# Performance work log

Measured on AMD Instinct MI355X. Metric: run time of the kernel, lower is better.

The kernel has to match this reference:

```python
import jax, jax.numpy as jnp
import numpy as np

N = 20000      # nodes
E = 320000     # edges (avg degree 16)
IN = 128       # in_size
H = 256        # layer_size
DEPTH = 2      # extra hidden layers
BN_EPS = 1e-5


def setup_inputs() -> dict:
    key = jax.random.key(0)
    ks = jax.random.split(key, 16)
    x = jax.random.normal(ks[0], (N, IN), jnp.float32)
    edge_index = jax.random.randint(ks[1], (2, E), 0, N)
    # first MLP layer: Linear(2*IN -> H) + BatchNorm1d(H) (inference stats)
    W0 = jax.random.normal(ks[2], (H, 2 * IN), jnp.float32) * 0.05
    b0 = jnp.zeros((H,), jnp.float32)
    g0 = jnp.ones((H,), jnp.float32)
    beta0 = jnp.zeros((H,), jnp.float32)
    m0 = jax.random.normal(ks[3], (H,), jnp.float32) * 0.1
    v0 = jax.random.uniform(ks[4], (H,), jnp.float32, 0.5, 1.5)
    # DEPTH repeated layers: Linear(H -> H) + BatchNorm1d(H)
    Ws = jax.random.normal(ks[5], (DEPTH, H, H), jnp.float32) * 0.05
    bs = jnp.zeros((DEPTH, H), jnp.float32)
    gs = jnp.ones((DEPTH, H), jnp.float32)
    betas = jnp.zeros((DEPTH, H), jnp.float32)
    ms = jax.random.normal(ks[6], (DEPTH, H), jnp.float32) * 0.1
    vs = jax.random.uniform(ks[7], (DEPTH, H), jnp.float32, 0.5, 1.5)
    return {"x": x, "edge_index": edge_index,
            "W0": W0, "b0": b0, "g0": g0, "beta0": beta0, "m0": m0, "v0": v0,
            "Ws": Ws, "bs": bs, "gs": gs, "betas": betas, "ms": ms, "vs": vs}


def _bn(h, g, b, m, v):
    # BatchNorm1d in inference mode (running stats)
    return (h - m) * (g * jax.lax.rsqrt(v + BN_EPS)) + b


def reference(x, edge_index, W0, b0, g0, beta0, m0, v0, Ws, bs, gs, betas, ms, vs):
    src = edge_index[0]  # x_j (source / neighbor)
    dst = edge_index[1]  # x_i (target), also scatter index
    # gather + concat: [E, 2*IN]
    h = jnp.concatenate([x[dst], x[src]], axis=-1)
    # edge MLP (dropout is identity in eval mode)
    h = jax.nn.selu(_bn(h @ W0.T + b0, g0, beta0, m0, v0))
    for i in range(DEPTH):
        h = jax.nn.selu(_bn(h @ Ws[i].T + bs[i], gs[i], betas[i], ms[i], vs[i]))
    # scatter-mean aggregation onto target nodes
    agg_sum = jax.ops.segment_sum(h, dst, num_segments=N)
    cnt = jax.ops.segment_sum(jnp.ones((E,), h.dtype), dst, num_segments=N)
    agg = agg_sum / jnp.maximum(cnt, 1.0)[:, None]
    return (agg, h)  # (aggregated node features, edge activations)
```

## Files before the change

### kernel.cpp

```cpp
#include <hip/hip_runtime.h>
#include <hip/hip_bf16.h>

#define IN_F 128
#define HF 256
#define BN_EPS 1e-5f
#define SELU_SCALE 1.0507009873554805f
#define SELU_ALPHA 1.6732632423543772f

typedef __attribute__((ext_vector_type(8))) _Float16 half8;
typedef __attribute__((ext_vector_type(2))) unsigned int u32x2;
typedef __attribute__((ext_vector_type(4))) float f32x4;

__device__ __forceinline__ short f2h(float f) {
    _Float16 h = (_Float16)f;
    return __builtin_bit_cast(short, h);
}

__device__ __forceinline__ float selu_f(float x) {
    const float SA = SELU_SCALE * SELU_ALPHA;
    float e = __expf(x);
    return x > 0.f ? SELU_SCALE * x : SA * e - SA;
}

__device__ __forceinline__ unsigned int pk2h(float a, float b) {
    return __builtin_bit_cast(unsigned int, __builtin_amdgcn_cvt_pkrtz(a, b));
}

__device__ __forceinline__ void gld_lds16(const void* g, void* l) {
    __builtin_amdgcn_global_load_lds(
        (const __attribute__((address_space(1))) unsigned int*)g,
        (__attribute__((address_space(3))) unsigned int*)l, 16, 0, 0);
}

__global__ void prep_kernel(const float* __restrict__ W0, const float* __restrict__ b0,
                            const float* __restrict__ g0, const float* __restrict__ beta0,
                            const float* __restrict__ m0, const float* __restrict__ v0,
                            const float* __restrict__ Ws, const float* __restrict__ bs,
                            const float* __restrict__ gs, const float* __restrict__ betas,
                            const float* __restrict__ ms, const float* __restrict__ vs,
                            unsigned short* __restrict__ Wf, float* __restrict__ biasArr) {
    int b = blockIdx.x;
    int layer = b >> 8;
    int n = b & 255;
    int k = threadIdx.x;
    const float *W, *bb, *g, *be, *m, *v;
    if (layer == 0) { W = W0; bb = b0; g = g0; be = beta0; m = m0; v = v0; }
    else {
        int i = layer - 1;
        W = Ws + (size_t)i * HF * HF; bb = bs + i * HF; g = gs + i * HF;
        be = betas + i * HF; m = ms + i * HF; v = vs + i * HF;
    }
    float s = g[n] * rsqrtf(v[n] + BN_EPS);
    int kk = k >> 5, kc = (k >> 3) & 3, j = k & 7;
    Wf[((((size_t)layer * 8 + kk) * 4 + kc) * 256 + n) * 8 + j] =
        (unsigned short)f2h(W[n * HF + k] * s);
    if (k == 0) biasArr[layer * HF + n] = (bb[n] - m[n]) * s + be[n];
}

__global__ void count_kernel(const int* __restrict__ dstI, int* __restrict__ cnt, int E) {
    int i = blockIdx.x * 256 + threadIdx.x;
    if (i < E) atomicAdd(cnt + dstI[i], 1);
}

__global__ void scan_local(const int* __restrict__ cnt, int* __restrict__ wrk,
                           int* __restrict__ btot, int n) {
    __shared__ int s[1024];
    int b = blockIdx.x, t = threadIdx.x, i = b * 1024 + t;
    int v = (i < n) ? cnt[i] : 0;
    s[t] = v;
    __syncthreads();
#pragma unroll
    for (int d = 1; d < 1024; d <<= 1) {
        int add = (t >= d) ? s[t - d] : 0;
        __syncthreads();
        s[t] += add;
        __syncthreads();
    }
    if (i < n) wrk[i] = s[t] - v;
    if (t == 1023) btot[b] = s[1023];
}
__global__ void scan_tops(int* __restrict__ btot, int nb) {
    if (threadIdx.x == 0) {
        int run = 0;
        for (int i = 0; i < nb; ++i) { int v = btot[i]; btot[i] = run; run += v; }
    }
}
__global__ void scan_add(int* __restrict__ wrk, const int* __restrict__ btot, int n) {
    int i = blockIdx.x * 1024 + threadIdx.x;
    if (i < n) wrk[i] += btot[blockIdx.x];
}

__global__ void scatter_kernel(const int* __restrict__ dstI, int* __restrict__ wrk,
                               int* __restrict__ perm, int E) {
    int i = blockIdx.x * 256 + threadIdx.x;
    if (i < E) {
        int p = atomicAdd(wrk + dstI[i], 1);
        perm[p] = i;
    }
}

__global__ void finalize_kernel(float* __restrict__ agg, const int* __restrict__ cnt) {
    int n = blockIdx.x;
    float c = fmaxf((float)cnt[n], 1.f);
    agg[(size_t)n * HF + threadIdx.x] = agg[(size_t)n * HF + threadIdx.x] / c;
}

__global__ __launch_bounds__(256, 3)
void fused_kernel(const float* __restrict__ x,
                  const int* __restrict__ dstI, const int* __restrict__ srcI,
                  const int* __restrict__ perm,
                  const unsigned char* __restrict__ Wfb,
                  const float* __restrict__ biasArr,
                  unsigned char* __restrict__ hB, float* __restrict__ agg) {
    __shared__ __align__(16) unsigned char lds[49152];
    __shared__ int peL[64];
    __shared__ int pdL[64];

    const int base = blockIdx.x * 64;
    const int t = threadIdx.x;
    const int lane = t & 63;
    const int w = t >> 6;
    const int lrow = lane & 15;
    const int lgrp = lane >> 4;

    auto stageB = [&](int L, int kk) {
        const unsigned char* src = Wfb + ((size_t)(L * 8 + kk) << 14);
        unsigned char* dstBase = lds + 32768 + w * 1024;
#pragma unroll
        for (int i = 0; i < 4; ++i)
            gld_lds16(src + (i * 256 + t) * 16, dstBase + i * 4096);
    };

    stageB(0, 0);

    {
        int r = t >> 2, q = t & 3;
        int e = perm[base + r];
        int idx = (q < 2 ? dstI : srcI)[e];
        const float* xr = x + (size_t)idx * IN_F + (q & 1) * 64;
        int swz = (r & 7) << 4;
#pragma unroll
        for (int u = 0; u < 16; ++u) {
            f32x4 v = *(const f32x4*)(xr + u * 4);
            u32x2 hv = {pk2h(v[0], v[1]), pk2h(v[2], v[3])};
            *(u32x2*)&lds[r * 512 + ((q * 128 + u * 8) ^ swz)] = hv;
        }
    }

    f32x4 acc[4][4];
    const f32x4 zero = {0.f, 0.f, 0.f, 0.f};

#pragma unroll
    for (int L = 0; L < 3; ++L) {
#pragma unroll
        for (int mi = 0; mi < 4; ++mi)
#pragma unroll
            for (int ni = 0; ni < 4; ++ni) acc[mi][ni] = zero;

#pragma unroll
        for (int kk = 0; kk < 8; ++kk) {
            __syncthreads();

            half8 af[4], bf[4];
#pragma unroll
            for (int mi = 0; mi < 4; ++mi) {
                int row = mi * 16 + lrow;
                af[mi] = *(const half8*)&lds[row * 512 +
                    ((kk * 64 + lgrp * 16) ^ ((row & 7) << 4))];
            }
#pragma unroll
            for (int ni = 0; ni < 4; ++ni)
                bf[ni] = *(const half8*)&lds[32768 + lgrp * 4096 +
                                             (w * 64 + ni * 16 + lrow) * 16];
            __syncthreads();

            if (kk < 7) stageB(L, kk + 1);
            else if (L < 2) stageB(L + 1, 0);

            if (L < 2) {
#pragma unroll
                for (int mi = 0; mi < 4; ++mi)
#pragma unroll
                    for (int ni = 0; ni < 4; ++ni)
                        acc[mi][ni] = __builtin_amdgcn_mfma_f32_16x16x32_f16(
                            bf[ni], af[mi], acc[mi][ni], 0, 0, 0);
            } else {
#pragma unroll
                for (int mi = 0; mi < 4; ++mi)
#pragma unroll
                    for (int ni = 0; ni < 4; ++ni)
                        acc[mi][ni] = __builtin_amdgcn_mfma_f32_16x16x32_f16(
                            af[mi], bf[ni], acc[mi][ni], 0, 0, 0);
            }
        }

        if (L < 2) {
#pragma unroll
            for (int ni = 0; ni < 4; ++ni) {
                f32x4 bv = *(const f32x4*)(biasArr + L * HF + w * 64 + ni * 16 + lgrp * 4);
#pragma unroll
                for (int mi = 0; mi < 4; ++mi) {
                    int row = mi * 16 + lrow;
                    float v0 = selu_f(acc[mi][ni][0] + bv[0]);
                    float v1 = selu_f(acc[mi][ni][1] + bv[1]);
                    float v2 = selu_f(acc[mi][ni][2] + bv[2]);
                    float v3 = selu_f(acc[mi][ni][3] + bv[3]);
                    u32x2 d = {pk2h(v0, v1), pk2h(v2, v3)};
                    *(u32x2*)&lds[row * 512 +
                        ((w * 128 + ni * 32 + lgrp * 8) ^ ((row & 7) << 4))] = d;
                }
            }
        } else {
            if (t < 64) {
                int e = perm[base + t];
                peL[t] = e;
                pdL[t] = dstI[e];
            }
            float bc[4];
#pragma unroll
            for (int ni = 0; ni < 4; ++ni) bc[ni] = biasArr[2 * HF + w * 64 + ni * 16 + lrow];
            unsigned char* EP = lds + 32768;
            int curD = -1;
            float carry = 0.f;
#pragma unroll
            for (int cc = 0; cc < 4; ++cc) {
                if (cc) __syncthreads();
#pragma unroll
                for (int ni = 0; ni < 4; ++ni)
#pragma unroll
                    for (int r = 0; r < 4; ++r) {
                        int er = lgrp * 4 + r;
                        int cg = w * 64 + ni * 16 + lrow;
                        float val = selu_f(acc[cc][ni][r] + bc[ni]);
                        *(float*)&EP[er * 1024 + ((cg * 4) ^ ((er & 7) << 4))] = val;
                    }
                __syncthreads();
#pragma unroll
                for (int i = 0; i < 4; ++i) {
                    int f = t + i * 256;
                    int row = f >> 6, ch = f & 63;
                    f32x4 v = *(const f32x4*)&EP[row * 1024 + ((ch * 16) ^ ((row & 7) << 4))];
                    *(f32x4*)(hB + (size_t)peL[cc * 16 + row] * 1024 + ch * 16) = v;
                }
#pragma unroll
                for (int r = 0; r < 16; ++r) {
                    float v = *(const float*)&EP[r * 1024 + ((t * 4) ^ ((r & 7) << 4))];
                    int d = pdL[cc * 16 + r];
                    if (d != curD) {
                        if (curD >= 0) atomicAdd(agg + (size_t)curD * HF + t, carry);
                        carry = 0.f;
                        curD = d;
                    }
                    carry += v;
                }
            }
            atomicAdd(agg + (size_t)curD * HF + t, carry);
        }
    }
}

extern "C" void kernel_launch(void* const* d_in, const int* in_sizes, int n_in,
                              void* d_out, int out_size, void* d_ws, size_t ws_size,
                              hipStream_t stream) {
    const float* x     = (const float*)d_in[0];
    const int*   ei    = (const int*)d_in[1];
    const float* W0    = (const float*)d_in[2];
    const float* b0    = (const float*)d_in[3];
    const float* g0    = (const float*)d_in[4];
    const float* beta0 = (const float*)d_in[5];
    const float* m0    = (const float*)d_in[6];
    const float* v0    = (const float*)d_in[7];
    const float* Ws    = (const float*)d_in[8];
    const float* bs    = (const float*)d_in[9];
    const float* gs    = (const float*)d_in[10];
    const float* betas = (const float*)d_in[11];
    const float* ms    = (const float*)d_in[12];
    const float* vs    = (const float*)d_in[13];

    const int Nn = in_sizes[0] / IN_F;
    const int E  = in_sizes[1] / 2;

    float* agg  = (float*)d_out;
    float* hptr = agg + (size_t)Nn * HF;

    char* wsb = (char*)d_ws;
    unsigned short* Wf = (unsigned short*)wsb;
    float* biasArr = (float*)(wsb + 393216);
    int* cnt  = (int*)(wsb + 396288);
    int* wrk  = (int*)(wsb + 476288);
    int* perm = (int*)(wsb + 556288);
    int* btot = (int*)agg;

    const int* srcI = ei;
    const int* dstI = ei + E;

    const int nScan = (Nn + 1023) / 1024;

    prep_kernel<<<3 * HF, HF, 0, stream>>>(W0, b0, g0, beta0, m0, v0,
                                           Ws, bs, gs, betas, ms, vs, Wf, biasArr);
    hipMemsetAsync(cnt, 0, (size_t)Nn * sizeof(int), stream);
    count_kernel<<<(E + 255) / 256, 256, 0, stream>>>(dstI, cnt, E);
    scan_local<<<nScan, 1024, 0, stream>>>(cnt, wrk, btot, Nn);
    scan_tops<<<1, 64, 0, stream>>>(btot, nScan);
    scan_add<<<nScan, 1024, 0, stream>>>(wrk, btot, Nn);
    hipMemsetAsync(agg, 0, (size_t)Nn * HF * sizeof(float), stream);
    scatter_kernel<<<(E + 255) / 256, 256, 0, stream>>>(dstI, wrk, perm, E);

    fused_kernel<<<E / 64, 256, 0, stream>>>(x, dstI, srcI, perm,
                                             (const unsigned char*)Wf, biasArr,
                                             (unsigned char*)hptr, agg);

    finalize_kernel<<<Nn, HF, 0, stream>>>(agg, cnt);
}
```

Baseline: 291.7 us.

## Double fused edge-MLP tile to 128 edges with 8 waves sharing weight slabs

Each block of the fused edge-MLP kernel now handles 128 edges with 512 threads arranged as a 2x4 wave grid, instead of 64 edges with 256 threads. Each staged weight slab in LDS now serves twice as many edge rows, which halves weight-staging traffic and barrier overhead per edge. LDS moves to 80 KB of dynamic shared memory. The epilogue loops over 8 chunks of 16 rows, and only the first 256 threads do the segmented atomic aggregation. The cost is fewer resident blocks per CU and larger blocks whose barriers stall more waves at once, which may reduce latency hiding for the gathers and atomics.

```diff
diff --git a/kernel.cpp b/kernel.cpp
--- a/kernel.cpp
+++ b/kernel.cpp
@@ -105,30 +105,31 @@
     agg[(size_t)n * HF + threadIdx.x] = agg[(size_t)n * HF + threadIdx.x] / c;
 }
 
-__global__ __launch_bounds__(256, 3)
+extern "C" __global__ __launch_bounds__(512, 4)
 void fused_kernel(const float* __restrict__ x,
                   const int* __restrict__ dstI, const int* __restrict__ srcI,
                   const int* __restrict__ perm,
                   const unsigned char* __restrict__ Wfb,
                   const float* __restrict__ biasArr,
                   unsigned char* __restrict__ hB, float* __restrict__ agg) {
-    __shared__ __align__(16) unsigned char lds[49152];
-    __shared__ int peL[64];
-    __shared__ int pdL[64];
-
-    const int base = blockIdx.x * 64;
+    extern __shared__ __align__(16) unsigned char lds[];
+    unsigned char* ldsB = lds + 65536;
+
+    const int base = blockIdx.x * 128;
     const int t = threadIdx.x;
     const int lane = t & 63;
     const int w = t >> 6;
+    const int wr = w >> 2;
+    const int wcol = w & 3;
     const int lrow = lane & 15;
     const int lgrp = lane >> 4;
 
     auto stageB = [&](int L, int kk) {
         const unsigned char* src = Wfb + ((size_t)(L * 8 + kk) << 14);
-        unsigned char* dstBase = lds + 32768 + w * 1024;
-#pragma unroll
-        for (int i = 0; i < 4; ++i)
-            gld_lds16(src + (i * 256 + t) * 16, dstBase + i * 4096);
+        unsigned char* dstBase = ldsB + w * 1024;
+#pragma unroll
+        for (int i = 0; i < 2; ++i)
+            gld_lds16(src + (i * 512 + t) * 16, dstBase + i * 8192);
     };
 
     stageB(0, 0);
@@ -164,14 +165,14 @@
             half8 af[4], bf[4];
 #pragma unroll
             for (int mi = 0; mi < 4; ++mi) {
-                int row = mi * 16 + lrow;
+                int row = wr * 64 + mi * 16 + lrow;
                 af[mi] = *(const half8*)&lds[row * 512 +
                     ((kk * 64 + lgrp * 16) ^ ((row & 7) << 4))];
             }
 #pragma unroll
             for (int ni = 0; ni < 4; ++ni)
-                bf[ni] = *(const half8*)&lds[32768 + lgrp * 4096 +
-                                             (w * 64 + ni * 16 + lrow) * 16];
+                bf[ni] = *(const half8*)&ldsB[lgrp * 4096 +
+                                              (wcol * 64 + ni * 16 + lrow) * 16];
             __syncthreads();
 
             if (kk < 7) stageB(L, kk + 1);
@@ -197,64 +198,73 @@
         if (L < 2) {
 #pragma unroll
             for (int ni = 0; ni < 4; ++ni) {
-                f32x4 bv = *(const f32x4*)(biasArr + L * HF + w * 64 + ni * 16 + lgrp * 4);
+                f32x4 bv = *(const f32x4*)(biasArr + L * HF + wcol * 64 + ni * 16 + lgrp * 4);
 #pragma unroll
                 for (int mi = 0; mi < 4; ++mi) {
-                    int row = mi * 16 + lrow;
+                    int row = wr * 64 + mi * 16 + lrow;
                     float v0 = selu_f(acc[mi][ni][0] + bv[0]);
                     float v1 = selu_f(acc[mi][ni][1] + bv[1]);
                     float v2 = selu_f(acc[mi][ni][2] + bv[2]);
                     float v3 = selu_f(acc[mi][ni][3] + bv[3]);
                     u32x2 d = {pk2h(v0, v1), pk2h(v2, v3)};
                     *(u32x2*)&lds[row * 512 +
-                        ((w * 128 + ni * 32 + lgrp * 8) ^ ((row & 7) << 4))] = d;
+                        ((wcol * 128 + ni * 32 + lgrp * 8) ^ ((row & 7) << 4))] = d;
                 }
             }
         } else {
-            if (t < 64) {
+            if (t < 128) {
                 int e = perm[base + t];
-                peL[t] = e;
-                pdL[t] = dstI[e];
-            }
+                ((int*)lds)[t] = e;
+                ((int*)lds)[128 + t] = dstI[e];
+            }
+            const int* peL = (const int*)lds;
+            const int* pdL = (const int*)lds + 128;
             float bc[4];
 #pragma unroll
-            for (int ni = 0; ni < 4; ++ni) bc[ni] = biasArr[2 * HF + w * 64 + ni * 16 + lrow];
-            unsigned char* EP = lds + 32768;
+            for (int ni = 0; ni < 4; ++ni)
+                bc[ni] = biasArr[2 * HF + wcol * 64 + ni * 16 + lrow];
+            unsigned char* EP = ldsB;
             int curD = -1;
             float carry = 0.f;
 #pragma unroll
-            for (int cc = 0; cc < 4; ++cc) {
+            for (int cc = 0; cc < 8; ++cc) {
                 if (cc) __syncthreads();
-#pragma unroll
-                for (int ni = 0; ni < 4; ++ni)
-#pragma unroll
-                    for (int r = 0; r < 4; ++r) {
-                        int er = lgrp * 4 + r;
-                        int cg = w * 64 + ni * 16 + lrow;
-                        float val = selu_f(acc[cc][ni][r] + bc[ni]);
-                        *(float*)&EP[er * 1024 + ((cg * 4) ^ ((er & 7) << 4))] = val;
-                    }
+                if (wr == (cc >> 2)) {
+                    int mi = cc & 3;
+#pragma unroll
+                    for (int ni = 0; ni < 4; ++ni)
+#pragma unroll
+                        for (int r = 0; r < 4; ++r) {
+                            int er = lgrp * 4 + r;
+                            int cg = wcol * 64 + ni * 16 + lrow;
+                            float val = selu_f(acc[mi][ni][r] + bc[ni]);
+                            *(float*)&EP[er * 1024 + ((cg * 4) ^ ((er & 7) << 4))] = val;
+                        }
+                }
                 __syncthreads();
 #pragma unroll
-                for (int i = 0; i < 4; ++i) {
-                    int f = t + i * 256;
+                for (int i = 0; i < 2; ++i) {
+                    int f = t + i * 512;
                     int row = f >> 6, ch = f & 63;
                     f32x4 v = *(const f32x4*)&EP[row * 1024 + ((ch * 16) ^ ((row & 7) << 4))];
                     *(f32x4*)(hB + (size_t)peL[cc * 16 + row] * 1024 + ch * 16) = v;
                 }
-#pragma unroll
-                for (int r = 0; r < 16; ++r) {
-                    float v = *(const float*)&EP[r * 1024 + ((t * 4) ^ ((r & 7) << 4))];
-                    int d = pdL[cc * 16 + r];
-                    if (d != curD) {
-                        if (curD >= 0) atomicAdd(agg + (size_t)curD * HF + t, carry);
-                        carry = 0.f;
-                        curD = d;
+                if (t < 256) {
+#pragma unroll
+                    for (int r = 0; r < 16; ++r) {
+                        float v = *(const float*)&EP[r * 1024 + ((t * 4) ^ ((r & 7) << 4))];
+                        int d = pdL[cc * 16 + r];
+                        if (d != curD) {
+                            if (curD >= 0) atomicAdd(agg + (size_t)curD * HF + t, carry);
+                            carry = 0.f;
+                            curD = d;
+                        }
+                        carry += v;
                     }
-                    carry += v;
                 }
             }
-            atomicAdd(agg + (size_t)curD * HF + t, carry);
+            if (t < 256 && curD >= 0)
+                atomicAdd(agg + (size_t)curD * HF + t, carry);
         }
     }
 }
@@ -295,6 +305,10 @@
     const int* dstI = ei + E;
 
     const int nScan = (Nn + 1023) / 1024;
+    const int LDS_BYTES = 81920;
+
+    hipFuncSetAttribute((const void*)fused_kernel,
+                        hipFuncAttributeMaxDynamicSharedMemorySize, LDS_BYTES);
 
     prep_kernel<<<3 * HF, HF, 0, stream>>>(W0, b0, g0, beta0, m0, v0,
                                            Ws, bs, gs, betas, ms, vs, Wf, biasArr);
@@ -306,9 +320,9 @@
     hipMemsetAsync(agg, 0, (size_t)Nn * HF * sizeof(float), stream);
     scatter_kernel<<<(E + 255) / 256, 256, 0, stream>>>(dstI, wrk, perm, E);
 
-    fused_kernel<<<E / 64, 256, 0, stream>>>(x, dstI, srcI, perm,
-                                             (const unsigned char*)Wf, biasArr,
-                                             (unsigned char*)hptr, agg);
+    fused_kernel<<<E / 128, 512, LDS_BYTES, stream>>>(x, dstI, srcI, perm,
+                                                      (const unsigned char*)Wf, biasArr,
+                                                      (unsigned char*)hptr, agg);
 
     finalize_kernel<<<Nn, HF, 0, stream>>>(agg, cnt);
 }
```

New measurement: 300.3 us. +2.9%, slower.

## Fold mean division into atomic scatter and prefetch A fragments across k-steps

Applied to the files above, without the earlier changes.

Computes the reciprocal of each node's edge count during the local scan, storing it in place of the count buffer. The fused kernel scales each partial sum by that reciprocal before its atomicAdd, which removes the separate finalize pass over the N×256 aggregation buffer. The k-loop also loads the next step's A-operand fragments from LDS before issuing the current MFMAs, to hide LDS latency. Each atomic now pays an extra global load of invA, and the double-buffered fragments raise register pressure, which may matter under launch_bounds(256,3).

```diff
diff --git a/kernel.cpp b/kernel.cpp
--- a/kernel.cpp
+++ b/kernel.cpp
@@ -62,7 +62,7 @@
     if (i < E) atomicAdd(cnt + dstI[i], 1);
 }
 
-__global__ void scan_local(const int* __restrict__ cnt, int* __restrict__ wrk,
+__global__ void scan_local(int* __restrict__ cnt, int* __restrict__ wrk,
                            int* __restrict__ btot, int n) {
     __shared__ int s[1024];
     int b = blockIdx.x, t = threadIdx.x, i = b * 1024 + t;
@@ -76,7 +76,10 @@
         s[t] += add;
         __syncthreads();
     }
-    if (i < n) wrk[i] = s[t] - v;
+    if (i < n) {
+        wrk[i] = s[t] - v;
+        ((float*)cnt)[i] = 1.f / fmaxf((float)v, 1.f);
+    }
     if (t == 1023) btot[b] = s[1023];
 }
 __global__ void scan_tops(int* __restrict__ btot, int nb) {
@@ -99,18 +102,13 @@
     }
 }
 
-__global__ void finalize_kernel(float* __restrict__ agg, const int* __restrict__ cnt) {
-    int n = blockIdx.x;
-    float c = fmaxf((float)cnt[n], 1.f);
-    agg[(size_t)n * HF + threadIdx.x] = agg[(size_t)n * HF + threadIdx.x] / c;
-}
-
 __global__ __launch_bounds__(256, 3)
 void fused_kernel(const float* __restrict__ x,
                   const int* __restrict__ dstI, const int* __restrict__ srcI,
                   const int* __restrict__ perm,
                   const unsigned char* __restrict__ Wfb,
                   const float* __restrict__ biasArr,
+                  const float* __restrict__ invA,
                   unsigned char* __restrict__ hB, float* __restrict__ agg) {
     __shared__ __align__(16) unsigned char lds[49152];
     __shared__ int peL[64];
@@ -130,6 +128,11 @@
         for (int i = 0; i < 4; ++i)
             gld_lds16(src + (i * 256 + t) * 16, dstBase + i * 4096);
     };
+    auto readA = [&](int kk, int mi) -> half8 {
+        int row = mi * 16 + lrow;
+        return *(const half8*)&lds[row * 512 +
+            ((kk * 64 + lgrp * 16) ^ ((row & 7) << 4))];
+    };
 
     stageB(0, 0);
 
@@ -157,17 +160,16 @@
 #pragma unroll
             for (int ni = 0; ni < 4; ++ni) acc[mi][ni] = zero;
 
+        half8 af_c[4], af_n[4];
 #pragma unroll
         for (int kk = 0; kk < 8; ++kk) {
             __syncthreads();
 
-            half8 af[4], bf[4];
-#pragma unroll
-            for (int mi = 0; mi < 4; ++mi) {
-                int row = mi * 16 + lrow;
-                af[mi] = *(const half8*)&lds[row * 512 +
-                    ((kk * 64 + lgrp * 16) ^ ((row & 7) << 4))];
-            }
+            if (kk == 0) {
+#pragma unroll
+                for (int mi = 0; mi < 4; ++mi) af_c[mi] = readA(0, mi);
+            }
+            half8 bf[4];
 #pragma unroll
             for (int ni = 0; ni < 4; ++ni)
                 bf[ni] = *(const half8*)&lds[32768 + lgrp * 4096 +
@@ -177,20 +179,29 @@
             if (kk < 7) stageB(L, kk + 1);
             else if (L < 2) stageB(L + 1, 0);
 
+            if (kk < 7) {
+#pragma unroll
+                for (int mi = 0; mi < 4; ++mi) af_n[mi] = readA(kk + 1, mi);
+            }
+
             if (L < 2) {
 #pragma unroll
                 for (int mi = 0; mi < 4; ++mi)
 #pragma unroll
                     for (int ni = 0; ni < 4; ++ni)
                         acc[mi][ni] = __builtin_amdgcn_mfma_f32_16x16x32_f16(
-                            bf[ni], af[mi], acc[mi][ni], 0, 0, 0);
+                            bf[ni], af_c[mi], acc[mi][ni], 0, 0, 0);
             } else {
 #pragma unroll
                 for (int mi = 0; mi < 4; ++mi)
 #pragma unroll
                     for (int ni = 0; ni < 4; ++ni)
                         acc[mi][ni] = __builtin_amdgcn_mfma_f32_16x16x32_f16(
-                            af[mi], bf[ni], acc[mi][ni], 0, 0, 0);
+                            af_c[mi], bf[ni], acc[mi][ni], 0, 0, 0);
+            }
+            if (kk < 7) {
+#pragma unroll
+                for (int mi = 0; mi < 4; ++mi) af_c[mi] = af_n[mi];
             }
         }
 
@@ -247,14 +258,15 @@
                     float v = *(const float*)&EP[r * 1024 + ((t * 4) ^ ((r & 7) << 4))];
                     int d = pdL[cc * 16 + r];
                     if (d != curD) {
-                        if (curD >= 0) atomicAdd(agg + (size_t)curD * HF + t, carry);
+                        if (curD >= 0)
+                            atomicAdd(agg + (size_t)curD * HF + t, carry * invA[curD]);
                         carry = 0.f;
                         curD = d;
                     }
                     carry += v;
                 }
             }
-            atomicAdd(agg + (size_t)curD * HF + t, carry);
+            atomicAdd(agg + (size_t)curD * HF + t, carry * invA[curD]);
         }
     }
 }
@@ -308,7 +320,6 @@
 
     fused_kernel<<<E / 64, 256, 0, stream>>>(x, dstI, srcI, perm,
                                              (const unsigned char*)Wf, biasArr,
+                                             (const float*)cnt,
                                              (unsigned char*)hptr, agg);
-
-    finalize_kernel<<<Nn, HF, 0, stream>>>(agg, cnt);
-}
+}
```

Result: faster. 271.7 us (-6.9%).
